# Performance work log

Measured on AMD Instinct MI355X. Metric: run time of the kernel, lower is better.

The kernel has to match this reference:

```python
import jax, jax.numpy as jnp
import numpy as np

B, N, D, K = 8, 2048, 256, 8192


def setup_inputs() -> dict:
    key = jax.random.key(0)
    k1, k2 = jax.random.split(key)
    x = jax.random.normal(k1, (B, N, D), dtype=jnp.float32)          # encoder output z_e (identity encoder)
    codebook = jax.random.normal(k2, (K, D), dtype=jnp.float32)      # nn.Parameter(codebook_size, codebook_dim)
    return {"x": x, "codebook": codebook}


def reference(x, codebook):
    z_e = x  # identity encoder
    # Squared Euclidean distances via matmul expansion: ||z||^2 - 2 z.c^T + ||c||^2 -> (B, N, K)
    z2 = jnp.sum(z_e * z_e, axis=-1, keepdims=True)                   # (B, N, 1)
    c2 = jnp.sum(codebook * codebook, axis=-1)                        # (K,)
    cross = jnp.einsum('bnd,kd->bnk', z_e, codebook)                  # (B, N, K)
    distances = z2 - 2.0 * cross + c2                                 # (B, N, K)
    indices = jnp.argmin(distances, axis=-1)                          # (B, N) int
    z_q = codebook[indices]                                           # gather -> (B, N, D)
    x_recon = z_q  # identity decoder
    return (x_recon, z_e, z_q, indices)
```

## Files before the change

### kernel.cpp

```cpp
#include <hip/hip_runtime.h>
#include <stdint.h>


#define M_ROWS 16384
#define D_DIM  256
#define K_CB   8192
#define KP     256
#define NSPLIT 16
#define BM 128
#define BN 128
#define BK 64
#define EPS 0.30f

typedef _Float16 half4v __attribute__((ext_vector_type(4)));
typedef _Float16 half8v __attribute__((ext_vector_type(8)));
typedef float    f32x4  __attribute__((ext_vector_type(4)));

__device__ __forceinline__ void gld_lds16(const void* g, void* l) {
  __builtin_amdgcn_global_load_lds((__attribute__((address_space(1))) void*)g,
                                   (__attribute__((address_space(3))) void*)l,
                                   16, 0, 0);
}

__global__ __launch_bounds__(256) void prep_x(const float* __restrict__ x,
                                              _Float16* __restrict__ Ap) {
  const int w = threadIdx.x >> 6, lane = threadIdx.x & 63;
  const int row = blockIdx.x * 4 + w;
  const f32x4 v = *(const f32x4*)(x + (size_t)row * D_DIM + lane * 4);
  half4v hi;
#pragma unroll
  for (int t = 0; t < 4; ++t) hi[t] = (_Float16)v[t];
  *(half4v*)(Ap + (size_t)row * KP + lane * 4) = hi;
}

__global__ __launch_bounds__(256) void prep_cb(const float* __restrict__ cb,
                                               _Float16* __restrict__ Bp,
                                               float* __restrict__ c2) {
  const int w = threadIdx.x >> 6, lane = threadIdx.x & 63;
  const int row = blockIdx.x * 4 + w;
  const f32x4 v = *(const f32x4*)(cb + (size_t)row * D_DIM + lane * 4);
  half4v hi;
  double s = 0.0;
#pragma unroll
  for (int t = 0; t < 4; ++t) {
    hi[t] = (_Float16)v[t];
    s += (double)v[t] * (double)v[t];
  }
  *(half4v*)(Bp + (size_t)row * KP + lane * 4) = hi;
#pragma unroll
  for (int m = 1; m < 64; m <<= 1) s += __shfl_xor(s, m, 64);
  if (lane == 0) c2[row] = (float)s;
}

__global__ __launch_bounds__(256, 2) void vq_main(const _Float16* __restrict__ Ap,
                                                  const _Float16* __restrict__ Bp,
                                                  const float* __restrict__ c2,
                                                  uint2* __restrict__ part) {
  __shared__ _Float16 As[BM * BK];
  __shared__ _Float16 Bs[BN * BK];
  __shared__ uint2 sred[BM * 2];

  const int tid  = threadIdx.x;
  const int w    = tid >> 6;
  const int lane = tid & 63;
  const int wm   = w >> 1;
  const int wn   = w & 1;

  const int rowBase = blockIdx.x * BM;
  const int nBase   = blockIdx.y * (K_CB / NSPLIT);

  const int stRow   = lane >> 3;
  const int stColH  = ((lane & 7) ^ stRow) * 8;

  const int fr = lane & 15;
  const int fq = lane >> 4;

  uint32_t t1[4][4], t2[4][4];
#pragma unroll
  for (int i = 0; i < 4; ++i)
#pragma unroll
    for (int r = 0; r < 4; ++r) { t1[i][r] = 0x7f7ffe00u; t2[i][r] = 0x7f7ffe00u; }

  for (int nit = 0; nit < (K_CB / NSPLIT) / BN; ++nit) {
    f32x4 acc[4][4];
#pragma unroll
    for (int i = 0; i < 4; ++i)
#pragma unroll
      for (int j = 0; j < 4; ++j) acc[i][j] = (f32x4){0.f, 0.f, 0.f, 0.f};

    for (int kt = 0; kt < KP / BK; ++kt) {
      const int kb = kt * BK;
#pragma unroll
      for (int ii = 0; ii < 4; ++ii) {
        const int rt = w * 32 + ii * 8 + stRow;
        gld_lds16(Ap + (size_t)(rowBase + rt) * KP + kb + stColH,
                  As + rt * BK + (lane & 7) * 8);
      }
#pragma unroll
      for (int ii = 0; ii < 4; ++ii) {
        const int rt = w * 32 + ii * 8 + stRow;
        gld_lds16(Bp + (size_t)(nBase + nit * BN + rt) * KP + kb + stColH,
                  Bs + rt * BK + (lane & 7) * 8);
      }
      __syncthreads();
#pragma unroll
      for (int ks = 0; ks < 2; ++ks) {
        half8v af[4], bf[4];
        const int xc = ((ks * 4 + fq) ^ (fr & 7)) * 8;
#pragma unroll
        for (int i = 0; i < 4; ++i)
          af[i] = *(const half8v*)(As + (wm * 64 + i * 16 + fr) * BK + xc);
#pragma unroll
        for (int j = 0; j < 4; ++j)
          bf[j] = *(const half8v*)(Bs + (wn * 64 + j * 16 + fr) * BK + xc);
#pragma unroll
        for (int i = 0; i < 4; ++i)
#pragma unroll
          for (int j = 0; j < 4; ++j)
            acc[i][j] = __builtin_amdgcn_mfma_f32_16x16x32_f16(af[i], bf[j],
                                                               acc[i][j], 0, 0, 0);
      }
      __syncthreads();
    }

#pragma unroll
    for (int j = 0; j < 4; ++j) {
      const int col9 = nit * BN + wn * 64 + j * 16 + fr;
      const float cv = c2[nBase + col9];
#pragma unroll
      for (int i = 0; i < 4; ++i)
#pragma unroll
        for (int r = 0; r < 4; ++r) {
          const float s = fmaf(-2.0f, acc[i][j][r], cv);
          const uint32_t p = (__float_as_uint(s) & ~511u) | (uint32_t)col9;
          const uint32_t hi = t1[i][r] > p ? t1[i][r] : p;
          t1[i][r] = t1[i][r] < p ? t1[i][r] : p;
          t2[i][r] = t2[i][r] < hi ? t2[i][r] : hi;
        }
    }
  }

#pragma unroll
  for (int i = 0; i < 4; ++i)
#pragma unroll
    for (int r = 0; r < 4; ++r) {
      uint32_t a1 = t1[i][r], a2 = t2[i][r];
#pragma unroll
      for (int m = 1; m < 16; m <<= 1) {
        const uint32_t o1 = __shfl_xor(a1, m, 64);
        const uint32_t o2 = __shfl_xor(a2, m, 64);
        const uint32_t hi = a1 > o1 ? a1 : o1;
        a1 = a1 < o1 ? a1 : o1;
        const uint32_t lo2 = a2 < o2 ? a2 : o2;
        a2 = lo2 < hi ? lo2 : hi;
      }
      if (fr == 0) {
        const int row = wm * 64 + i * 16 + fq * 4 + r;
        sred[row * 2 + wn] = make_uint2(a1, a2);
      }
    }
  __syncthreads();
  if (tid < BM) {
    const uint2 a = sred[tid * 2 + 0], b = sred[tid * 2 + 1];
    const uint32_t hi = a.x > b.x ? a.x : b.x;
    const uint32_t m1 = a.x < b.x ? a.x : b.x;
    const uint32_t lo2 = a.y < b.y ? a.y : b.y;
    const uint32_t m2 = lo2 < hi ? lo2 : hi;
    part[(size_t)(rowBase + tid) * NSPLIT + blockIdx.y] = make_uint2(m1, m2);
  }
}

__global__ __launch_bounds__(256) void vq_merge(const uint2* __restrict__ part,
                                                const float* __restrict__ x,
                                                const float* __restrict__ cb,
                                                float* __restrict__ out) {
  const int w = threadIdx.x >> 6, lane = threadIdx.x & 63;
  const int row = blockIdx.x * 4 + w;

  uint32_t pk = 0x7f7ffe00u;
  int gidx = 0x7fffffff;
  if (lane < 32) {
    const uint2 pp = part[(size_t)row * NSPLIT + (lane >> 1)];
    pk = (lane & 1) ? pp.y : pp.x;
    gidx = (lane >> 1) * (K_CB / NSPLIT) + (int)(pk & 511u);
  }
  uint32_t pmin = pk;
#pragma unroll
  for (int m = 1; m < 64; m <<= 1) {
    const uint32_t o = __shfl_xor(pmin, m, 64);
    pmin = pmin < o ? pmin : o;
  }
  const float vmin = __uint_as_float(pmin & ~511u);
  const float vme  = __uint_as_float(pk & ~511u);
  const unsigned long long mask = __ballot(lane < 32 && vme <= vmin + EPS);

  const f32x4 xv = *(const f32x4*)(x + (size_t)row * D_DIM + lane * 4);

  int winner;
  if (__popcll(mask) == 1) {
    winner = __shfl(gidx, __ffsll((long long)mask) - 1, 64);
  } else {
    double bestd = 1.0e300;
    int bidx = 0x7fffffff;
    unsigned long long mm = mask;
    while (mm) {
      const int q = __ffsll((long long)mm) - 1;
      mm &= mm - 1;
      const int ci = __shfl(gidx, q, 64);
      const f32x4 cv = *(const f32x4*)(cb + (size_t)ci * D_DIM + lane * 4);
      double s = 0.0;
#pragma unroll
      for (int t = 0; t < 4; ++t) {
        const double dx = (double)xv[t] - (double)cv[t];
        s += dx * dx;
      }
#pragma unroll
      for (int m = 1; m < 64; m <<= 1) s += __shfl_xor(s, m, 64);
      if (s < bestd || (s == bestd && ci < bidx)) { bestd = s; bidx = ci; }
    }
    winner = bidx;
  }

  float* out_recon = out;
  float* out_ze    = out + (size_t)M_ROWS * D_DIM;
  float* out_zq    = out + 2 * (size_t)M_ROWS * D_DIM;
  float* out_idx   = out + 3 * (size_t)M_ROWS * D_DIM;

  const f32x4 cv = *(const f32x4*)(cb + (size_t)winner * D_DIM + lane * 4);
  *(f32x4*)(out_recon + (size_t)row * D_DIM + lane * 4) = cv;
  *(f32x4*)(out_zq    + (size_t)row * D_DIM + lane * 4) = cv;
  *(f32x4*)(out_ze    + (size_t)row * D_DIM + lane * 4) = xv;
  if (lane == 0) out_idx[row] = (float)winner;
}

extern "C" void kernel_launch(void* const* d_in, const int* in_sizes, int n_in,
                              void* d_out, int out_size, void* d_ws, size_t ws_size,
                              hipStream_t stream) {
  const float* x  = (const float*)d_in[0];
  const float* cb = (const float*)d_in[1];
  float* out = (float*)d_out;

  char* ws = (char*)d_ws;
  float*     c2   = (float*)ws;
  uint2*     part = (uint2*)(ws + 32768);
  _Float16*  Ap   = (_Float16*)(ws + 32768 + 2097152);
  _Float16*  Bp   = Ap + (size_t)M_ROWS * KP;
  if (ws_size < (size_t)(32768 + 2097152 + 8388608 + 4194304)) return;

  prep_x  <<<dim3(M_ROWS / 4), dim3(256), 0, stream>>>(x, Ap);
  prep_cb <<<dim3(K_CB / 4),   dim3(256), 0, stream>>>(cb, Bp, c2);
  vq_main <<<dim3(M_ROWS / BM, NSPLIT), dim3(256), 0, stream>>>(Ap, Bp, c2, part);
  vq_merge<<<dim3(M_ROWS / 4), dim3(256), 0, stream>>>(part, x, cb, out);
}
```

Baseline: 186.5 us.

## Switch distance GEMM from fp16 to fp8 scaled MFMA with wider rescoring margin

```diff
diff --git a/kernel.cpp b/kernel.cpp
--- a/kernel.cpp
+++ b/kernel.cpp
@@ -5,16 +5,14 @@
 #define M_ROWS 16384
 #define D_DIM  256
 #define K_CB   8192
-#define KP     256
 #define NSPLIT 16
 #define BM 128
 #define BN 128
-#define BK 64
-#define EPS 0.30f
-
-typedef _Float16 half4v __attribute__((ext_vector_type(4)));
-typedef _Float16 half8v __attribute__((ext_vector_type(8)));
-typedef float    f32x4  __attribute__((ext_vector_type(4)));
+#define EPS 12.0f
+
+typedef float f32x4 __attribute__((ext_vector_type(4)));
+typedef int   int4v __attribute__((ext_vector_type(4)));
+typedef int   int8v __attribute__((ext_vector_type(8)));
 
 __device__ __forceinline__ void gld_lds16(const void* g, void* l) {
   __builtin_amdgcn_global_load_lds((__attribute__((address_space(1))) void*)g,
@@ -22,42 +20,50 @@
                                    16, 0, 0);
 }
 
-__global__ __launch_bounds__(256) void prep_x(const float* __restrict__ x,
-                                              _Float16* __restrict__ Ap) {
+__device__ __forceinline__ uint32_t fp8x4(const f32x4 v) {
+  int p = __builtin_amdgcn_cvt_pk_fp8_f32(v[0], v[1], 0, false);
+  p = __builtin_amdgcn_cvt_pk_fp8_f32(v[2], v[3], p, true);
+  return (uint32_t)p;
+}
+
+__global__ __launch_bounds__(256) void prep(const float* __restrict__ x,
+                                            const float* __restrict__ cb,
+                                            uint8_t* __restrict__ Ap,
+                                            uint8_t* __restrict__ Bp,
+                                            float* __restrict__ c2) {
   const int w = threadIdx.x >> 6, lane = threadIdx.x & 63;
-  const int row = blockIdx.x * 4 + w;
-  const f32x4 v = *(const f32x4*)(x + (size_t)row * D_DIM + lane * 4);
-  half4v hi;
-#pragma unroll
-  for (int t = 0; t < 4; ++t) hi[t] = (_Float16)v[t];
-  *(half4v*)(Ap + (size_t)row * KP + lane * 4) = hi;
-}
-
-__global__ __launch_bounds__(256) void prep_cb(const float* __restrict__ cb,
-                                               _Float16* __restrict__ Bp,
-                                               float* __restrict__ c2) {
-  const int w = threadIdx.x >> 6, lane = threadIdx.x & 63;
-  const int row = blockIdx.x * 4 + w;
-  const f32x4 v = *(const f32x4*)(cb + (size_t)row * D_DIM + lane * 4);
-  half4v hi;
-  double s = 0.0;
-#pragma unroll
-  for (int t = 0; t < 4; ++t) {
-    hi[t] = (_Float16)v[t];
-    s += (double)v[t] * (double)v[t];
-  }
-  *(half4v*)(Bp + (size_t)row * KP + lane * 4) = hi;
-#pragma unroll
-  for (int m = 1; m < 64; m <<= 1) s += __shfl_xor(s, m, 64);
-  if (lane == 0) c2[row] = (float)s;
-}
-
-__global__ __launch_bounds__(256, 2) void vq_main(const _Float16* __restrict__ Ap,
-                                                  const _Float16* __restrict__ Bp,
+  if (blockIdx.x < M_ROWS / 4) {
+    const int row = blockIdx.x * 4 + w;
+    const f32x4 v = *(const f32x4*)(x + (size_t)row * D_DIM + lane * 4);
+    *(uint32_t*)(Ap + (size_t)row * D_DIM + lane * 4) = fp8x4(v);
+  } else {
+    const int row = (blockIdx.x - M_ROWS / 4) * 4 + w;
+    const f32x4 v = *(const f32x4*)(cb + (size_t)row * D_DIM + lane * 4);
+    *(uint32_t*)(Bp + (size_t)row * D_DIM + lane * 4) = fp8x4(v);
+    double s = 0.0;
+#pragma unroll
+    for (int t = 0; t < 4; ++t) s += (double)v[t] * (double)v[t];
+#pragma unroll
+    for (int m = 1; m < 64; m <<= 1) s += __shfl_xor(s, m, 64);
+    if (lane == 0) c2[row] = (float)s;
+  }
+}
+
+__device__ __forceinline__ int8v frag8(const uint8_t* rowp, int fq, int x7) {
+  const int4v lo = *(const int4v*)(rowp + (((fq * 2)     ^ x7) << 4));
+  const int4v hi = *(const int4v*)(rowp + (((fq * 2 + 1) ^ x7) << 4));
+  int8v r;
+#pragma unroll
+  for (int t = 0; t < 4; ++t) { r[t] = lo[t]; r[4 + t] = hi[t]; }
+  return r;
+}
+
+__global__ __launch_bounds__(256, 3) void vq_main(const uint8_t* __restrict__ Ap,
+                                                  const uint8_t* __restrict__ Bp,
                                                   const float* __restrict__ c2,
                                                   uint2* __restrict__ part) {
-  __shared__ _Float16 As[BM * BK];
-  __shared__ _Float16 Bs[BN * BK];
+  __shared__ uint8_t As[BM * 128];
+  __shared__ uint8_t Bs[BN * 128];
   __shared__ uint2 sred[BM * 2];
 
   const int tid  = threadIdx.x;
@@ -69,11 +75,12 @@
   const int rowBase = blockIdx.x * BM;
   const int nBase   = blockIdx.y * (K_CB / NSPLIT);
 
-  const int stRow   = lane >> 3;
-  const int stColH  = ((lane & 7) ^ stRow) * 8;
+  const int stRow  = lane >> 3;
+  const int stColB = ((lane & 7) ^ stRow) * 16;
 
   const int fr = lane & 15;
   const int fq = lane >> 4;
+  const int x7 = fr & 7;
 
   uint32_t t1[4][4], t2[4][4];
 #pragma unroll
@@ -88,37 +95,34 @@
 #pragma unroll
       for (int j = 0; j < 4; ++j) acc[i][j] = (f32x4){0.f, 0.f, 0.f, 0.f};
 
-    for (int kt = 0; kt < KP / BK; ++kt) {
-      const int kb = kt * BK;
+#pragma unroll
+    for (int kh = 0; kh < 2; ++kh) {
+      const int kb = kh * 128;
 #pragma unroll
       for (int ii = 0; ii < 4; ++ii) {
         const int rt = w * 32 + ii * 8 + stRow;
-        gld_lds16(Ap + (size_t)(rowBase + rt) * KP + kb + stColH,
-                  As + rt * BK + (lane & 7) * 8);
+        gld_lds16(Ap + (size_t)(rowBase + rt) * D_DIM + kb + stColB,
+                  As + rt * 128 + (lane & 7) * 16);
       }
 #pragma unroll
       for (int ii = 0; ii < 4; ++ii) {
         const int rt = w * 32 + ii * 8 + stRow;
-        gld_lds16(Bp + (size_t)(nBase + nit * BN + rt) * KP + kb + stColH,
-                  Bs + rt * BK + (lane & 7) * 8);
+        gld_lds16(Bp + (size_t)(nBase + nit * BN + rt) * D_DIM + kb + stColB,
+                  Bs + rt * 128 + (lane & 7) * 16);
       }
       __syncthreads();
-#pragma unroll
-      for (int ks = 0; ks < 2; ++ks) {
-        half8v af[4], bf[4];
-        const int xc = ((ks * 4 + fq) ^ (fr & 7)) * 8;
-#pragma unroll
-        for (int i = 0; i < 4; ++i)
-          af[i] = *(const half8v*)(As + (wm * 64 + i * 16 + fr) * BK + xc);
+      int8v bf[4];
+#pragma unroll
+      for (int j = 0; j < 4; ++j)
+        bf[j] = frag8(Bs + (wn * 64 + j * 16 + fr) * 128, fq, x7);
+#pragma unroll
+      for (int i = 0; i < 4; ++i) {
+        const int8v av = frag8(As + (wm * 64 + i * 16 + fr) * 128, fq, x7);
 #pragma unroll
         for (int j = 0; j < 4; ++j)
-          bf[j] = *(const half8v*)(Bs + (wn * 64 + j * 16 + fr) * BK + xc);
-#pragma unroll
-        for (int i = 0; i < 4; ++i)
-#pragma unroll
-          for (int j = 0; j < 4; ++j)
-            acc[i][j] = __builtin_amdgcn_mfma_f32_16x16x32_f16(af[i], bf[j],
-                                                               acc[i][j], 0, 0, 0);
+          acc[i][j] = __builtin_amdgcn_mfma_scale_f32_16x16x128_f8f6f4(
+              av, bf[j], acc[i][j], 0, 0,
+              0, 0x7f7f7f7f, 0, 0x7f7f7f7f);
       }
       __syncthreads();
     }
@@ -126,7 +130,7 @@
 #pragma unroll
     for (int j = 0; j < 4; ++j) {
       const int col9 = nit * BN + wn * 64 + j * 16 + fr;
-      const float cv = c2[nBase + col9];
+      const float cv = c2[nBase + col9] + 1024.0f;
 #pragma unroll
       for (int i = 0; i < 4; ++i)
 #pragma unroll
@@ -241,14 +245,13 @@
   float* out = (float*)d_out;
 
   char* ws = (char*)d_ws;
-  float*     c2   = (float*)ws;
-  uint2*     part = (uint2*)(ws + 32768);
-  _Float16*  Ap   = (_Float16*)(ws + 32768 + 2097152);
-  _Float16*  Bp   = Ap + (size_t)M_ROWS * KP;
-  if (ws_size < (size_t)(32768 + 2097152 + 8388608 + 4194304)) return;
-
-  prep_x  <<<dim3(M_ROWS / 4), dim3(256), 0, stream>>>(x, Ap);
-  prep_cb <<<dim3(K_CB / 4),   dim3(256), 0, stream>>>(cb, Bp, c2);
+  float*    c2   = (float*)ws;
+  uint2*    part = (uint2*)(ws + 32768);
+  uint8_t*  Ap   = (uint8_t*)(ws + 32768 + 2097152);
+  uint8_t*  Bp   = Ap + (size_t)M_ROWS * D_DIM;
+  if (ws_size < (size_t)(32768 + 2097152 + 4194304 + 2097152)) return;
+
+  prep    <<<dim3(M_ROWS / 4 + K_CB / 4), dim3(256), 0, stream>>>(x, cb, Ap, Bp, c2);
   vq_main <<<dim3(M_ROWS / BM, NSPLIT), dim3(256), 0, stream>>>(Ap, Bp, c2, part);
   vq_merge<<<dim3(M_ROWS / 4), dim3(256), 0, stream>>>(part, x, cb, out);
 }
```

New measurement: 189.7 us. No clear change (+1.7%).
